# Kernel optimization log

Measured on AMD Instinct MI355X. Metric: run time of the kernel, lower is better.

## Reference

```python
import jax, jax.numpy as jnp
import numpy as np

B, S, DIM, H = 2, 1024, 512, 8
HD = DIM // H          # head_dim = 64
EPS = 1e-5
W_SCALE = 0.02         # keep activations stable (relu(gate)^2 downstream)


def causal_fft_conv(filters, x):
    """filters: [S, H]; x: [b, h, s, d]. Linear (full) convolution along s,
    truncated to the first s samples — identical to
    jax.scipy.signal.convolve(filter, seq, method='fft')[:s] per (h, d)."""
    s = x.shape[2]
    n = 2 * s  # >= 2s-1, enough for linear convolution
    f = jnp.fft.rfft(filters.T, n=n, axis=-1)          # [h, nf]
    xf = jnp.fft.rfft(x, n=n, axis=2)                  # [b, h, nf, d]
    y = jnp.fft.irfft(xf * f[None, :, :, None], n=n, axis=2)
    return y[:, :, :s, :]


def setup_inputs() -> dict:
    key = jax.random.key(0)
    ks = jax.random.split(key, 8)
    inp = {
        "x": jax.random.normal(ks[0], (B, S, DIM), dtype=jnp.float32),
        "spectral_basis": jax.random.normal(ks[1], (S, H), dtype=jnp.float32),
        "wq_w": jax.random.normal(ks[2], (DIM, DIM), dtype=jnp.float32) * W_SCALE,
        "wq_b": jnp.zeros((DIM,), jnp.float32),
        "wk_w": jax.random.normal(ks[3], (DIM, DIM), dtype=jnp.float32) * W_SCALE,
        "wk_b": jnp.zeros((DIM,), jnp.float32),
        "wv_w": jax.random.normal(ks[4], (DIM, DIM), dtype=jnp.float32) * W_SCALE,
        "wv_b": jnp.zeros((DIM,), jnp.float32),
        "wo_w": jax.random.normal(ks[5], (DIM, DIM), dtype=jnp.float32) * W_SCALE,
        "wo_b": jnp.zeros((DIM,), jnp.float32),
        "gate_w": jax.random.normal(ks[6], (HD * HD, 1), dtype=jnp.float32) * W_SCALE,
        "gate_b": jnp.zeros((1,), jnp.float32),
    }
    return inp


def reference(x, spectral_basis, wq_w, wq_b, wk_w, wk_b, wv_w, wv_b,
              wo_w, wo_b, gate_w, gate_b):
    b, s, dim = x.shape
    h = spectral_basis.shape[1]
    hd = dim // h

    def proj(w, bias):
        return (x @ w + bias).reshape(b, s, h, hd).transpose(0, 2, 1, 3)  # [b,h,s,d]

    q = proj(wq_w, wq_b)
    k = proj(wk_w, wk_b) / jnp.sqrt(jnp.asarray(hd, x.dtype))
    v = proj(wv_w, wv_b)

    k = causal_fft_conv(spectral_basis, k)
    v = causal_fft_conv(spectral_basis, v)

    # Outer-product state per step: [b, h, s, d, e]
    Z = jnp.einsum('bhsd,bhse->bhsde', v, k)

    # gate_proj: Dense(1) over flattened (d, e)
    gl = jnp.einsum('bhsde,de->bhs', Z, gate_w.reshape(hd, hd)) + gate_b[0]
    gates = jax.nn.relu(gl) ** 2 + EPS                 # [b, h, s]
    gates = gates[..., None, None]                     # [b, h, s, 1, 1]

    # Associative scan with (+, +) == cumulative sums along s
    cum_gZ = jnp.cumsum(gates * Z, axis=2)             # [b, h, s, d, e]
    cum_g = jnp.cumsum(gates, axis=2)                  # [b, h, s, 1, 1]
    attn = cum_gZ / (cum_g + EPS)

    out = jnp.einsum('bhsd,bhsde->bhse', q, attn)      # [b, h, s, e]
    nrm = jnp.linalg.norm(out, axis=3, keepdims=True)
    out = out / jnp.maximum(nrm, EPS)
    out = out.transpose(0, 2, 1, 3).reshape(b, s, dim)
    return out @ wo_w + wo_b
```

## Files before the change

### kernel.cpp

```cpp
#include <hip/hip_runtime.h>
#include <math.h>

#define B 2
#define S 1024
#define DIM 512
#define H 8
#define HD 64
#define EPS 1e-5f

typedef __attribute__((ext_vector_type(8))) short bf16x8;
typedef __attribute__((ext_vector_type(4))) float f32x4;
typedef unsigned short u16;
typedef unsigned int u32;

__device__ inline u16 f2bf(float f) {
    unsigned int u = __float_as_uint(f);
    return (u16)((u + 0x7FFF + ((u >> 16) & 1)) >> 16);
}
__device__ inline float bf2f(u16 v) {
    return __uint_as_float(((unsigned int)v) << 16);
}
__device__ inline void split2(float x, u16* hi, u16* lo) {
    u16 h = f2bf(x);
    *hi = h;
    *lo = f2bf(x - bf2f(h));
}
#define MFMA16(a, b, c) __builtin_amdgcn_mfma_f32_16x16x32_bf16((a), (b), (c), 0, 0, 0)

__device__ inline void gl16(const void* g, void* l) {
    __builtin_amdgcn_global_load_lds((const __attribute__((address_space(1))) u32*)g,
                                     (__attribute__((address_space(3))) u32*)l, 16, 0, 0);
}

__global__ void prep_k(const float* __restrict__ x,
                       const float* __restrict__ wq, const float* __restrict__ wk,
                       const float* __restrict__ wv, const float* __restrict__ wo,
                       const float* __restrict__ filt, const float* __restrict__ gw,
                       u16* __restrict__ xh, u16* __restrict__ xl,
                       u16* __restrict__ wqkvh, u16* __restrict__ wqkvl,
                       u16* __restrict__ woh, u16* __restrict__ wol,
                       u16* __restrict__ Th, u16* __restrict__ Tl,
                       u16* __restrict__ Gh, u16* __restrict__ Gl,
                       float* __restrict__ Kacc, int* __restrict__ cnt) {
    int bid = blockIdx.x, tid = threadIdx.x;
    __shared__ float T[64][65];
    if (bid < 1024) {
        int i = bid * 256 + tid;
        float4 v = ((const float4*)x)[i];
        ushort4 h, l;
        split2(v.x, &h.x, &l.x); split2(v.y, &h.y, &l.y);
        split2(v.z, &h.z, &l.z); split2(v.w, &h.w, &l.w);
        ((ushort4*)xh)[i] = h; ((ushort4*)xl)[i] = l;
    } else if (bid < 1280) {
        int q = bid - 1024;
        int z = q >> 6, rem = q & 63;
        int k0 = (rem >> 3) * 64, n0 = (rem & 7) * 64;
        const float* src = (z == 0) ? wq : (z == 1) ? wk : (z == 2) ? wv : wo;
        u16* dh = (z < 3) ? (wqkvh + (size_t)z * 512 * 512) : woh;
        u16* dl = (z < 3) ? (wqkvl + (size_t)z * 512 * 512) : wol;
        #pragma unroll
        for (int p = 0; p < 16; ++p) {
            int i = tid + 256 * p; int r = i >> 6, c = i & 63;
            T[r][c] = src[(k0 + r) * 512 + n0 + c];
        }
        __syncthreads();
        #pragma unroll
        for (int p = 0; p < 16; ++p) {
            int i = tid + 256 * p; int r = i >> 6, c = i & 63;
            size_t di = (size_t)(n0 + r) * 512 + k0 + c;
            split2(T[c][r], &dh[di], &dl[di]);
        }
    } else if (bid < 1408) {
        int q = bid - 1280;
        int h = q >> 4, delta = q & 15;
        size_t base = ((size_t)h * 16 + delta) << 12;
        #pragma unroll
        for (int p = 0; p < 16; ++p) {
            int i = tid + 256 * p;
            int t = i >> 6, s = i & 63;
            int idx = delta * 64 + t - s;
            float v = (idx >= 0 && idx < S) ? filt[idx * H + h] : 0.f;
            split2(v, &Th[base + i], &Tl[base + i]);
        }
    } else if (bid < 1920) {
        int i = (bid - 1408) * 256 + tid;
        float4 z4 = make_float4(0.f, 0.f, 0.f, 0.f);
        float4* dst = (float4*)Kacc;
        dst[i] = z4;
        dst[i + 131072] = z4;
        dst[i + 262144] = z4;
        dst[i + 393216] = z4;
    } else {
        if (tid < 16) cnt[tid] = 0;
        #pragma unroll
        for (int p = 0; p < 16; ++p) {
            int i = tid + 256 * p;
            split2(gw[i], &Gh[i], &Gl[i]);
        }
    }
}

template<int TN, int MODE>
__global__ __launch_bounds__(TN * 4) void gemm3k(
    const u16* __restrict__ Ah, const u16* __restrict__ Al,
    const u16* __restrict__ Bh, const u16* __restrict__ Bl,
    int N,
    const float* __restrict__ b0, const float* __restrict__ b1, const float* __restrict__ b2,
    float* __restrict__ outf,
    u16* __restrict__ qh, u16* __restrict__ ql,
    u16* __restrict__ kth, u16* __restrict__ ktl,
    u16* __restrict__ vth, u16* __restrict__ vtl)
{
    const int NT = TN * 4;
    __shared__ __align__(16) u16 LAh[64 * 64], LAl[64 * 64];
    __shared__ __align__(16) u16 LBh[TN * 64], LBl[TN * 64];
    int tid = threadIdx.x, l = tid & 63, wid = tid >> 6;
    int wm = wid & 1, wn = wid >> 1;
    int m0 = blockIdx.x * 64, n0 = blockIdx.y * TN;
    const u16* Abh = Ah + (size_t)m0 * 512;
    const u16* Abl = Al + (size_t)m0 * 512;
    const u16* Bbh = Bh + (size_t)n0 * 512;
    const u16* Bbl = Bl + (size_t)n0 * 512;
    int wbase = tid & ~63;
    f32x4 acc[2][2] = {};
    for (int k0s = 0; k0s < 8; ++k0s) {
        int k0 = k0s * 64;
        __syncthreads();
        #pragma unroll
        for (int i0 = 0; i0 < 512; i0 += NT) {
            int i = i0 + tid;
            int row = i >> 3, csw = (i & 7) ^ (row & 7);
            gl16(Abh + (size_t)row * 512 + k0 + csw * 8, LAh + (size_t)(i0 + wbase) * 8);
            gl16(Abl + (size_t)row * 512 + k0 + csw * 8, LAl + (size_t)(i0 + wbase) * 8);
        }
        #pragma unroll
        for (int i0 = 0; i0 < TN * 8; i0 += NT) {
            int i = i0 + tid;
            int row = i >> 3, csw = (i & 7) ^ (row & 7);
            gl16(Bbh + (size_t)row * 512 + k0 + csw * 8, LBh + (size_t)(i0 + wbase) * 8);
            gl16(Bbl + (size_t)row * 512 + k0 + csw * 8, LBl + (size_t)(i0 + wbase) * 8);
        }
        __syncthreads();
        #pragma unroll
        for (int kc = 0; kc < 2; ++kc) {
            bf16x8 ah[2], al[2], bh8[2], bl8[2];
            #pragma unroll
            for (int mi = 0; mi < 2; ++mi) {
                int ar = wm * 32 + mi * 16 + (l & 15);
                int ci = (kc * 4 + (l >> 4)) ^ (ar & 7);
                ah[mi] = *(const bf16x8*)(LAh + ar * 64 + ci * 8);
                al[mi] = *(const bf16x8*)(LAl + ar * 64 + ci * 8);
            }
            #pragma unroll
            for (int ni = 0; ni < 2; ++ni) {
                int br = wn * 32 + ni * 16 + (l & 15);
                int ci = (kc * 4 + (l >> 4)) ^ (br & 7);
                bh8[ni] = *(const bf16x8*)(LBh + br * 64 + ci * 8);
                bl8[ni] = *(const bf16x8*)(LBl + br * 64 + ci * 8);
            }
            #pragma unroll
            for (int mi = 0; mi < 2; ++mi)
                #pragma unroll
                for (int ni = 0; ni < 2; ++ni) {
                    acc[mi][ni] = MFMA16(ah[mi], bh8[ni], acc[mi][ni]);
                    acc[mi][ni] = MFMA16(ah[mi], bl8[ni], acc[mi][ni]);
                    acc[mi][ni] = MFMA16(al[mi], bh8[ni], acc[mi][ni]);
                }
        }
    }
    #pragma unroll
    for (int mi = 0; mi < 2; ++mi) {
        #pragma unroll
        for (int ni = 0; ni < 2; ++ni) {
            #pragma unroll
            for (int r = 0; r < 4; ++r) {
                int m = m0 + wm * 32 + mi * 16 + 4 * (l >> 4) + r;
                int n = n0 + wn * 32 + ni * 16 + (l & 15);
                float val = acc[mi][ni][r];
                if (MODE == 0) {
                    outf[(size_t)m * N + n] = val + b0[n];
                } else {
                    int bb = m >> 10, s = m & 1023;
                    int which = n >> 9, nn = n & 511;
                    int hh = nn >> 6, d = nn & 63;
                    int bh = bb * 8 + hh;
                    if (which == 0) {
                        val += b0[nn];
                        size_t di = ((size_t)bh * 1024 + s) * 64 + d;
                        split2(val, &qh[di], &ql[di]);
                    } else if (which == 1) {
                        val = (val + b1[nn]) * 0.125f;
                        size_t di = ((size_t)bh * 64 + d) * 1024 + s;
                        split2(val, &kth[di], &ktl[di]);
                    } else {
                        val += b2[nn];
                        size_t di = ((size_t)bh * 64 + d) * 1024 + s;
                        split2(val, &vth[di], &vtl[di]);
                    }
                }
            }
        }
    }
}

__global__ __launch_bounds__(256) void conv_part(
    const u16* __restrict__ kth, const u16* __restrict__ ktl,
    const u16* __restrict__ vth, const u16* __restrict__ vtl,
    const u16* __restrict__ Th, const u16* __restrict__ Tl,
    float* __restrict__ Kacc, float* __restrict__ Vacc)
{
    int jid = blockIdx.x, bh = blockIdx.y, h = bh & 7;
    int which = blockIdx.z;
    const u16* dhp = which ? vth : kth;
    const u16* dlp = which ? vtl : ktl;
    float* accg = which ? Vacc : Kacc;
    int tb, ch;
    if (jid < 4)       { tb = jid; ch = 0; }
    else if (jid < 12) { int q = jid - 4;  tb = 4 + (q >> 1); ch = q & 1; }
    else if (jid < 24) { int q = jid - 12; int d3 = q / 3; tb = 8 + d3; ch = q - 3 * d3; }
    else               { int q = jid - 24; tb = 12 + (q >> 2); ch = q & 3; }
    int sb0 = ch * 4, sb1 = min(sb0 + 4, tb + 1);
    int tid = threadIdx.x, wv = tid >> 6, l = tid & 63;
    __shared__ __align__(16) u16 Ash[4096], Asl[4096];
    __shared__ __align__(16) u16 Dsh[4096], Dsl[4096];
    f32x4 aD[4] = {};
    const size_t base = (size_t)bh * 64 * 1024;
    for (int sb = sb0; sb < sb1; ++sb) {
        __syncthreads();
        size_t tba = ((size_t)h * 16 + (tb - sb)) << 12;
        #pragma unroll
        for (int j = 0; j < 2; ++j) {
            int row = (j * 4 + wv) * 8 + (l >> 3);
            int csw = (l & 7) ^ (row & 7);
            int lo = (j * 4 + wv) * 512;
            gl16(Th + tba + row * 64 + csw * 8, Ash + lo);
            gl16(Tl + tba + row * 64 + csw * 8, Asl + lo);
            size_t gb = base + (size_t)row * 1024 + sb * 64 + csw * 8;
            gl16(dhp + gb, Dsh + lo);
            gl16(dlp + gb, Dsl + lo);
        }
        __syncthreads();
        #pragma unroll
        for (int seg = 0; seg < 3; ++seg) {
            const u16* Ase = (seg < 2) ? Ash : Asl;
            const u16* Dse = (seg == 1) ? Dsl : Dsh;
            #pragma unroll
            for (int kc = 0; kc < 2; ++kc) {
                int ar = 16 * wv + (l & 15);
                int acb = (kc * 64 + (l >> 4) * 16) ^ ((ar & 7) << 4);
                bf16x8 a = *(const bf16x8*)((const char*)(Ase + ar * 64) + acb);
                #pragma unroll
                for (int cf = 0; cf < 4; ++cf) {
                    int br = cf * 16 + (l & 15);
                    int bcb = (kc * 64 + (l >> 4) * 16) ^ ((br & 7) << 4);
                    bf16x8 bd = *(const bf16x8*)((const char*)(Dse + br * 64) + bcb);
                    aD[cf] = MFMA16(a, bd, aD[cf]);
                }
            }
        }
    }
    #pragma unroll
    for (int cf = 0; cf < 4; ++cf) {
        #pragma unroll
        for (int r = 0; r < 4; ++r) {
            int tl_ = 16 * wv + 4 * (l >> 4) + r;
            int d = cf * 16 + (l & 15);
            size_t oi = ((size_t)bh * 1024 + tb * 64 + tl_) * 64 + d;
            atomicAdd(&accg[oi], aD[cf][r]);
        }
    }
}

__global__ void conv_fin(const float* __restrict__ Kacc, const float* __restrict__ Vacc,
                         const u16* __restrict__ Gh, const u16* __restrict__ Gl,
                         const float* __restrict__ gb,
                         u16* __restrict__ kcth, u16* __restrict__ kctl,
                         u16* __restrict__ vcrh, u16* __restrict__ vcrl,
                         u16* __restrict__ vcth, u16* __restrict__ vctl,
                         float* __restrict__ g, float* __restrict__ cumg,
                         int* __restrict__ cnt) {
    int sc = blockIdx.x, bh = blockIdx.y;
    int tid = threadIdx.x, tx = tid & 63, ty = tid >> 6;
    int w = ty, l = tx;
    __shared__ float Kt[64][65], Vt[64][65];
    __shared__ float wtot[4];
    __shared__ int lastFlag;
    for (int i = tid; i < 4096; i += 256) {
        int r = i >> 6, c = i & 63;
        Kt[r][c] = Kacc[(((size_t)bh * 1024) + sc * 64 + r) * 64 + c];
        Vt[r][c] = Vacc[(((size_t)bh * 1024) + sc * 64 + r) * 64 + c];
    }
    __syncthreads();
    f32x4 tac[4] = {};
    #pragma unroll
    for (int kc = 0; kc < 2; ++kc) {
        int ar = 16 * w + (l & 15);
        int ac = kc * 32 + (l >> 4) * 8;
        bf16x8 ah, al;
        #pragma unroll
        for (int q = 0; q < 8; ++q) {
            float kv = Kt[ar][ac + q];
            u16 hi = f2bf(kv);
            ah[q] = (short)hi;
            al[q] = (short)f2bf(kv - bf2f(hi));
        }
        #pragma unroll
        for (int cf = 0; cf < 4; ++cf) {
            int br = cf * 16 + (l & 15);
            bf16x8 gh8 = *(const bf16x8*)&Gh[br * 64 + ac];
            bf16x8 gl8 = *(const bf16x8*)&Gl[br * 64 + ac];
            tac[cf] = MFMA16(ah, gh8, tac[cf]);
            tac[cf] = MFMA16(ah, gl8, tac[cf]);
            tac[cf] = MFMA16(al, gh8, tac[cf]);
        }
    }
    float gbias = gb[0];
    #pragma unroll
    for (int r = 0; r < 4; ++r) {
        int row = 16 * w + 4 * (l >> 4) + r;
        float pr = 0.f;
        #pragma unroll
        for (int cf = 0; cf < 4; ++cf) {
            int d = cf * 16 + (l & 15);
            pr += tac[cf][r] * Vt[row][d];
        }
        #pragma unroll
        for (int off = 1; off < 16; off <<= 1) pr += __shfl_xor(pr, off);
        if ((l & 15) == 0) {
            float gg = fmaxf(pr + gbias, 0.f);
            g[(size_t)bh * 1024 + sc * 64 + row] = gg * gg + EPS;
        }
    }
    #pragma unroll
    for (int it = 0; it < 16; ++it) {
        int r = it * 4 + ty;
        size_t ri = ((size_t)bh * 1024 + sc * 64 + r) * 64 + tx;
        split2(Vt[r][tx], &vcrh[ri], &vcrl[ri]);
    }
    #pragma unroll
    for (int it = 0; it < 16; ++it) {
        int d = it * 4 + ty;
        size_t ti = ((size_t)bh * 64 + d) * 1024 + sc * 64 + tx;
        split2(Kt[tx][d], &kcth[ti], &kctl[ti]);
        split2(Vt[tx][d], &vcth[ti], &vctl[ti]);
    }
    __threadfence();
    if (tid == 0) lastFlag = (atomicAdd(&cnt[bh], 1) == 15) ? 1 : 0;
    __syncthreads();
    if (lastFlag) {
        __threadfence();
        int ll = tid & 63, wv = tid >> 6;
        float4 v = ((const float4*)(g + (size_t)bh * 1024))[tid];
        float p0 = v.x, p1 = p0 + v.y, p2 = p1 + v.z, p3 = p2 + v.w;
        float t = p3, scn = t;
        #pragma unroll
        for (int off = 1; off < 64; off <<= 1) {
            float u = __shfl_up(scn, off);
            if (ll >= off) scn += u;
        }
        if (ll == 63) wtot[wv] = scn;
        __syncthreads();
        float bse = scn - t;
        for (int w2 = 0; w2 < wv; ++w2) bse += wtot[w2];
        float4 o = make_float4(bse + p0, bse + p1, bse + p2, bse + p3);
        ((float4*)(cumg + (size_t)bh * 1024))[tid] = o;
    }
}

__global__ void states_mfma(const u16* __restrict__ kcth, const u16* __restrict__ kctl,
                            const u16* __restrict__ vcth, const u16* __restrict__ vctl,
                            const float* __restrict__ g, float* __restrict__ Mst) {
    int j = blockIdx.x, bh = blockIdx.y;
    int tid = threadIdx.x, w = tid >> 6, l = tid & 63;
    __shared__ __align__(16) u16 Ash[64][72], Asl[64][72], Bsh[64][72], Bsl[64][72];
    __shared__ float gs[64];
    if (tid < 64) gs[tid] = g[(size_t)bh * 1024 + j * 64 + tid];
    __syncthreads();
    #pragma unroll
    for (int p = 0; p < 2; ++p) {
        int i = tid + 256 * p; int r = i >> 3, c8 = (i & 7) * 8;
        bf16x8 kh8 = *(const bf16x8*)&kcth[((size_t)bh * 64 + r) * 1024 + j * 64 + c8];
        bf16x8 kl8 = *(const bf16x8*)&kctl[((size_t)bh * 64 + r) * 1024 + j * 64 + c8];
        #pragma unroll
        for (int q = 0; q < 8; ++q) {
            float f = (bf2f((u16)kh8[q]) + bf2f((u16)kl8[q])) * gs[c8 + q];
            split2(f, &Ash[r][c8 + q], &Asl[r][c8 + q]);
        }
        *(bf16x8*)&Bsh[r][c8] = *(const bf16x8*)&vcth[((size_t)bh * 64 + r) * 1024 + j * 64 + c8];
        *(bf16x8*)&Bsl[r][c8] = *(const bf16x8*)&vctl[((size_t)bh * 64 + r) * 1024 + j * 64 + c8];
    }
    __syncthreads();
    f32x4 acc[4] = {};
    #pragma unroll
    for (int kc = 0; kc < 2; ++kc) {
        int ar = 16 * w + (l & 15), ac = kc * 32 + (l >> 4) * 8;
        bf16x8 ah = *(const bf16x8*)&Ash[ar][ac];
        bf16x8 al = *(const bf16x8*)&Asl[ar][ac];
        #pragma unroll
        for (int cf = 0; cf < 4; ++cf) {
            int br = cf * 16 + (l & 15);
            bf16x8 bh_ = *(const bf16x8*)&Bsh[br][ac];
            bf16x8 bl_ = *(const bf16x8*)&Bsl[br][ac];
            acc[cf] = MFMA16(ah, bh_, acc[cf]);
            acc[cf] = MFMA16(ah, bl_, acc[cf]);
            acc[cf] = MFMA16(al, bh_, acc[cf]);
        }
    }
    #pragma unroll
    for (int cf = 0; cf < 4; ++cf) {
        #pragma unroll
        for (int r = 0; r < 4; ++r) {
            int e = 16 * w + 4 * (l >> 4) + r;
            int d = cf * 16 + (l & 15);
            Mst[(((size_t)bh * 16 + j) * 64 + e) * 64 + d] = acc[cf][r];
        }
    }
}

__global__ void attn_mfma(const u16* __restrict__ qh, const u16* __restrict__ ql,
                          const float* __restrict__ Mst,
                          const u16* __restrict__ vcrh, const u16* __restrict__ vcrl,
                          const u16* __restrict__ kcth, const u16* __restrict__ kctl,
                          const float* __restrict__ g, const float* __restrict__ cumg,
                          u16* __restrict__ yh, u16* __restrict__ yl) {
    int tb = blockIdx.x, bh = blockIdx.y;
    int b = bh >> 3, h = bh & 7;
    int tid = threadIdx.x, w = tid >> 6, l = tid & 63;
    __shared__ __align__(16) u16 buf[6][64][72];
    __shared__ float gl_s[64], cg_s[64];
    float pref[16];
    #pragma unroll
    for (int p = 0; p < 16; ++p) pref[p] = 0.f;
    for (int j = 0; j < tb; ++j) {
        const float* Mb = Mst + ((size_t)(bh * 16 + j)) * 4096;
        #pragma unroll
        for (int p = 0; p < 16; ++p) pref[p] += Mb[tid + 256 * p];
    }
    #pragma unroll
    for (int p = 0; p < 2; ++p) {
        int i = tid + 256 * p; int r = i >> 3, c8 = (i & 7) * 8;
        size_t rowi = ((size_t)bh * 1024 + tb * 64 + r) * 64 + c8;
        *(bf16x8*)&buf[0][r][c8] = *(const bf16x8*)&qh[rowi];
        *(bf16x8*)&buf[1][r][c8] = *(const bf16x8*)&ql[rowi];
        *(bf16x8*)&buf[4][r][c8] = *(const bf16x8*)&vcrh[rowi];
        *(bf16x8*)&buf[5][r][c8] = *(const bf16x8*)&vcrl[rowi];
    }
    #pragma unroll
    for (int p = 0; p < 16; ++p) {
        int pos = tid + 256 * p;
        int r = pos >> 6, c = pos & 63;
        split2(pref[p], &buf[2][r][c], &buf[3][r][c]);
    }
    if (tid < 64) {
        gl_s[tid] = g[(size_t)bh * 1024 + tb * 64 + tid];
        cg_s[tid] = cumg[(size_t)bh * 1024 + tb * 64 + tid];
    }
    __syncthreads();
    f32x4 o[4] = {}, sc[4] = {};
    #pragma unroll
    for (int kc = 0; kc < 2; ++kc) {
        int ar = 16 * w + (l & 15), ac = kc * 32 + (l >> 4) * 8;
        bf16x8 ah = *(const bf16x8*)&buf[0][ar][ac];
        bf16x8 al = *(const bf16x8*)&buf[1][ar][ac];
        #pragma unroll
        for (int cf = 0; cf < 4; ++cf) {
            int br = cf * 16 + (l & 15);
            bf16x8 bph = *(const bf16x8*)&buf[2][br][ac];
            bf16x8 bpl = *(const bf16x8*)&buf[3][br][ac];
            bf16x8 bvh = *(const bf16x8*)&buf[4][br][ac];
            bf16x8 bvl = *(const bf16x8*)&buf[5][br][ac];
            o[cf] = MFMA16(ah, bph, o[cf]);
            o[cf] = MFMA16(ah, bpl, o[cf]);
            o[cf] = MFMA16(al, bph, o[cf]);
            sc[cf] = MFMA16(ah, bvh, sc[cf]);
            sc[cf] = MFMA16(ah, bvl, sc[cf]);
            sc[cf] = MFMA16(al, bvh, sc[cf]);
        }
    }
    __syncthreads();
    #pragma unroll
    for (int cf = 0; cf < 4; ++cf) {
        int s = cf * 16 + (l & 15);
        float gsv = gl_s[s];
        #pragma unroll
        for (int r = 0; r < 4; ++r) {
            int t = 16 * w + 4 * (l >> 4) + r;
            float v = (s <= t) ? sc[cf][r] * gsv : 0.f;
            split2(v, &buf[2][t][s], &buf[3][t][s]);
        }
    }
    #pragma unroll
    for (int p = 0; p < 2; ++p) {
        int i = tid + 256 * p; int r = i >> 3, c8 = (i & 7) * 8;
        size_t ti = ((size_t)bh * 64 + r) * 1024 + tb * 64 + c8;
        *(bf16x8*)&buf[4][r][c8] = *(const bf16x8*)&kcth[ti];
        *(bf16x8*)&buf[5][r][c8] = *(const bf16x8*)&kctl[ti];
    }
    __syncthreads();
    #pragma unroll
    for (int kc = 0; kc < 2; ++kc) {
        int ar = 16 * w + (l & 15), ac = kc * 32 + (l >> 4) * 8;
        bf16x8 ah = *(const bf16x8*)&buf[2][ar][ac];
        bf16x8 al = *(const bf16x8*)&buf[3][ar][ac];
        #pragma unroll
        for (int cf = 0; cf < 4; ++cf) {
            int br = cf * 16 + (l & 15);
            bf16x8 bh_ = *(const bf16x8*)&buf[4][br][ac];
            bf16x8 bl_ = *(const bf16x8*)&buf[5][br][ac];
            o[cf] = MFMA16(ah, bh_, o[cf]);
            o[cf] = MFMA16(ah, bl_, o[cf]);
            o[cf] = MFMA16(al, bh_, o[cf]);
        }
    }
    #pragma unroll
    for (int r = 0; r < 4; ++r) {
        int tl_ = 16 * w + 4 * (l >> 4) + r;
        float inv = 1.f / (cg_s[tl_] + EPS);
        float vv[4]; float sq = 0.f;
        #pragma unroll
        for (int cf = 0; cf < 4; ++cf) { vv[cf] = o[cf][r] * inv; sq += vv[cf] * vv[cf]; }
        #pragma unroll
        for (int off = 1; off < 16; off <<= 1) sq += __shfl_xor(sq, off);
        float scale = 1.f / fmaxf(sqrtf(sq), EPS);
        int tg = tb * 64 + tl_;
        #pragma unroll
        for (int cf = 0; cf < 4; ++cf) {
            int e = cf * 16 + (l & 15);
            size_t yi = ((size_t)b * 1024 + tg) * 512 + h * 64 + e;
            split2(vv[cf] * scale, &yh[yi], &yl[yi]);
        }
    }
}

extern "C" void kernel_launch(void* const* d_in, const int* in_sizes, int n_in,
                              void* d_out, int out_size, void* d_ws, size_t ws_size,
                              hipStream_t stream) {
    const float* x    = (const float*)d_in[0];
    const float* sbas = (const float*)d_in[1];
    const float* wq_w = (const float*)d_in[2];
    const float* wq_b = (const float*)d_in[3];
    const float* wk_w = (const float*)d_in[4];
    const float* wk_b = (const float*)d_in[5];
    const float* wv_w = (const float*)d_in[6];
    const float* wv_b = (const float*)d_in[7];
    const float* wo_w = (const float*)d_in[8];
    const float* wo_b = (const float*)d_in[9];
    const float* gw   = (const float*)d_in[10];
    const float* gb   = (const float*)d_in[11];
    float* out = (float*)d_out;

    char* p = (char*)d_ws;
    auto carve = [&](size_t bytes) { char* r = p; p += (bytes + 255) & ~(size_t)255; return r; };
    const size_t T2 = (size_t)2048 * 512 * 2;
    u16* xh = (u16*)carve(T2);      u16* xl = (u16*)carve(T2);
    u16* wqkvh = (u16*)carve((size_t)1536 * 512 * 2);
    u16* wqkvl = (u16*)carve((size_t)1536 * 512 * 2);
    u16* woh = (u16*)carve((size_t)512 * 512 * 2);
    u16* wol = (u16*)carve((size_t)512 * 512 * 2);
    u16* qh_ = (u16*)carve(T2);     u16* ql_ = (u16*)carve(T2);
    u16* kth_ = (u16*)carve(T2);    u16* ktl_ = (u16*)carve(T2);
    u16* vth_ = (u16*)carve(T2);    u16* vtl_ = (u16*)carve(T2);
    u16* Tth = (u16*)carve((size_t)8 * 16 * 4096 * 2);
    u16* Ttl = (u16*)carve((size_t)8 * 16 * 4096 * 2);
    u16* Gh_ = (u16*)carve(4096 * 2);
    u16* Gl_ = (u16*)carve(4096 * 2);
    float* Kacc = (float*)carve((size_t)16 * 1024 * 64 * 4);
    float* Vacc = (float*)carve((size_t)16 * 1024 * 64 * 4);
    u16* kcth_ = (u16*)carve(T2);   u16* kctl_ = (u16*)carve(T2);
    u16* vcrh_ = (u16*)carve(T2);   u16* vcrl_ = (u16*)carve(T2);
    u16* vcth_ = (u16*)carve(T2);   u16* vctl_ = (u16*)carve(T2);
    float* gbuf = (float*)carve((size_t)16 * 1024 * 4);
    float* cumg = (float*)carve((size_t)16 * 1024 * 4);
    float* Mst  = (float*)carve((size_t)16 * 16 * 4096 * 4);
    u16* yh_ = (u16*)carve(T2);     u16* yl_ = (u16*)carve(T2);
    int* cnt  = (int*)carve(64 * 4);

    prep_k<<<1921, 256, 0, stream>>>(x, wq_w, wk_w, wv_w, wo_w, sbas, gw,
                                     xh, xl, wqkvh, wqkvl, woh, wol, Tth, Ttl,
                                     Gh_, Gl_, Kacc, cnt);
    gemm3k<128, 1><<<dim3(32, 12), 512, 0, stream>>>(xh, xl, wqkvh, wqkvl, 1536,
                                                     wq_b, wk_b, wv_b, nullptr,
                                                     qh_, ql_, kth_, ktl_, vth_, vtl_);
    conv_part<<<dim3(40, 16, 2), 256, 0, stream>>>(kth_, ktl_, vth_, vtl_, Tth, Ttl, Kacc, Vacc);
    conv_fin<<<dim3(16, 16), 256, 0, stream>>>(Kacc, Vacc, Gh_, Gl_, gb,
                                               kcth_, kctl_, vcrh_, vcrl_, vcth_, vctl_,
                                               gbuf, cumg, cnt);
    states_mfma<<<dim3(16, 16), 256, 0, stream>>>(kcth_, kctl_, vcth_, vctl_, gbuf, Mst);
    attn_mfma<<<dim3(16, 16), 256, 0, stream>>>(qh_, ql_, Mst, vcrh_, vcrl_,
                                                kcth_, kctl_, gbuf, cumg, yh_, yl_);
    gemm3k<64, 0><<<dim3(32, 8), 256, 0, stream>>>(yh_, yl_, woh, wol, 512,
                                                   wo_b, nullptr, nullptr, out,
                                                   nullptr, nullptr, nullptr, nullptr, nullptr, nullptr);
}
```

Baseline: 191.1 us.

## Fuse per-chunk state computation into conv_fin and widen block to 512 threads

The states_mfma kernel is folded into conv_fin, which now computes the gated K^T V chunk state straight from the fp32 K/V tiles already held in shared memory. This removes one kernel launch and the global re-read of the split bf16 K/V arrays. The block grows to 512 threads so the gate projection and the state MFMAs are split across two column halves, with partial gate sums combined through shared memory. In exchange, each thread does more bf16 hi/lo splitting in registers, and the last-block cumulative-sum path has to guard threads beyond 256.

```diff
diff --git a/kernel.cpp b/kernel.cpp
--- a/kernel.cpp
+++ b/kernel.cpp
@@ -271,30 +271,34 @@
     }
 }
 
-__global__ void conv_fin(const float* __restrict__ Kacc, const float* __restrict__ Vacc,
-                         const u16* __restrict__ Gh, const u16* __restrict__ Gl,
-                         const float* __restrict__ gb,
-                         u16* __restrict__ kcth, u16* __restrict__ kctl,
-                         u16* __restrict__ vcrh, u16* __restrict__ vcrl,
-                         u16* __restrict__ vcth, u16* __restrict__ vctl,
-                         float* __restrict__ g, float* __restrict__ cumg,
-                         int* __restrict__ cnt) {
+__global__ __launch_bounds__(512) void conv_fin(
+        const float* __restrict__ Kacc, const float* __restrict__ Vacc,
+        const u16* __restrict__ Gh, const u16* __restrict__ Gl,
+        const float* __restrict__ gb,
+        u16* __restrict__ kcth, u16* __restrict__ kctl,
+        u16* __restrict__ vcrh, u16* __restrict__ vcrl,
+        u16* __restrict__ vcth, u16* __restrict__ vctl,
+        float* __restrict__ g, float* __restrict__ cumg,
+        float* __restrict__ Mst, int* __restrict__ cnt) {
     int sc = blockIdx.x, bh = blockIdx.y;
-    int tid = threadIdx.x, tx = tid & 63, ty = tid >> 6;
-    int w = ty, l = tx;
+    int tid = threadIdx.x, l = tid & 63;
+    int w = tid >> 6;
+    int rg = w & 3, chh = w >> 2;
     __shared__ float Kt[64][65], Vt[64][65];
+    __shared__ float pg[2][64];
+    __shared__ float gsh[64];
     __shared__ float wtot[4];
     __shared__ int lastFlag;
-    for (int i = tid; i < 4096; i += 256) {
+    for (int i = tid; i < 4096; i += 512) {
         int r = i >> 6, c = i & 63;
         Kt[r][c] = Kacc[(((size_t)bh * 1024) + sc * 64 + r) * 64 + c];
         Vt[r][c] = Vacc[(((size_t)bh * 1024) + sc * 64 + r) * 64 + c];
     }
     __syncthreads();
-    f32x4 tac[4] = {};
+    f32x4 tac[2] = {};
     #pragma unroll
     for (int kc = 0; kc < 2; ++kc) {
-        int ar = 16 * w + (l & 15);
+        int ar = 16 * rg + (l & 15);
         int ac = kc * 32 + (l >> 4) * 8;
         bf16x8 ah, al;
         #pragma unroll
@@ -305,52 +309,98 @@
             al[q] = (short)f2bf(kv - bf2f(hi));
         }
         #pragma unroll
-        for (int cf = 0; cf < 4; ++cf) {
-            int br = cf * 16 + (l & 15);
+        for (int cfi = 0; cfi < 2; ++cfi) {
+            int br = (chh * 2 + cfi) * 16 + (l & 15);
             bf16x8 gh8 = *(const bf16x8*)&Gh[br * 64 + ac];
             bf16x8 gl8 = *(const bf16x8*)&Gl[br * 64 + ac];
-            tac[cf] = MFMA16(ah, gh8, tac[cf]);
-            tac[cf] = MFMA16(ah, gl8, tac[cf]);
-            tac[cf] = MFMA16(al, gh8, tac[cf]);
-        }
-    }
+            tac[cfi] = MFMA16(ah, gh8, tac[cfi]);
+            tac[cfi] = MFMA16(ah, gl8, tac[cfi]);
+            tac[cfi] = MFMA16(al, gh8, tac[cfi]);
+        }
+    }
+    #pragma unroll
+    for (int r = 0; r < 4; ++r) {
+        int row = 16 * rg + 4 * (l >> 4) + r;
+        float pr = 0.f;
+        #pragma unroll
+        for (int cfi = 0; cfi < 2; ++cfi) {
+            int d = (chh * 2 + cfi) * 16 + (l & 15);
+            pr += tac[cfi][r] * Vt[row][d];
+        }
+        #pragma unroll
+        for (int off = 1; off < 16; off <<= 1) pr += __shfl_xor(pr, off);
+        if ((l & 15) == 0) pg[chh][row] = pr;
+    }
+    __syncthreads();
     float gbias = gb[0];
-    #pragma unroll
-    for (int r = 0; r < 4; ++r) {
-        int row = 16 * w + 4 * (l >> 4) + r;
-        float pr = 0.f;
-        #pragma unroll
-        for (int cf = 0; cf < 4; ++cf) {
-            int d = cf * 16 + (l & 15);
-            pr += tac[cf][r] * Vt[row][d];
-        }
-        #pragma unroll
-        for (int off = 1; off < 16; off <<= 1) pr += __shfl_xor(pr, off);
-        if ((l & 15) == 0) {
-            float gg = fmaxf(pr + gbias, 0.f);
-            g[(size_t)bh * 1024 + sc * 64 + row] = gg * gg + EPS;
-        }
-    }
-    #pragma unroll
-    for (int it = 0; it < 16; ++it) {
-        int r = it * 4 + ty;
-        size_t ri = ((size_t)bh * 1024 + sc * 64 + r) * 64 + tx;
-        split2(Vt[r][tx], &vcrh[ri], &vcrl[ri]);
-    }
-    #pragma unroll
-    for (int it = 0; it < 16; ++it) {
-        int d = it * 4 + ty;
-        size_t ti = ((size_t)bh * 64 + d) * 1024 + sc * 64 + tx;
-        split2(Kt[tx][d], &kcth[ti], &kctl[ti]);
-        split2(Vt[tx][d], &vcth[ti], &vctl[ti]);
+    if (tid < 64) {
+        float gg = fmaxf(pg[0][tid] + pg[1][tid] + gbias, 0.f);
+        float gv = gg * gg + EPS;
+        gsh[tid] = gv;
+        g[(size_t)bh * 1024 + sc * 64 + tid] = gv;
+    }
+    __syncthreads();
+    {
+        f32x4 mac[2] = {};
+        #pragma unroll
+        for (int kc = 0; kc < 2; ++kc) {
+            int are = 16 * rg + (l & 15);
+            int ac = kc * 32 + (l >> 4) * 8;
+            bf16x8 ah, al;
+            #pragma unroll
+            for (int q = 0; q < 8; ++q) {
+                float f = gsh[ac + q] * Kt[ac + q][are];
+                u16 hi = f2bf(f);
+                ah[q] = (short)hi;
+                al[q] = (short)f2bf(f - bf2f(hi));
+            }
+            #pragma unroll
+            for (int cfi = 0; cfi < 2; ++cfi) {
+                int brd = (chh * 2 + cfi) * 16 + (l & 15);
+                bf16x8 bh8, bl8;
+                #pragma unroll
+                for (int q = 0; q < 8; ++q) {
+                    float f = Vt[ac + q][brd];
+                    u16 hi = f2bf(f);
+                    bh8[q] = (short)hi;
+                    bl8[q] = (short)f2bf(f - bf2f(hi));
+                }
+                mac[cfi] = MFMA16(ah, bh8, mac[cfi]);
+                mac[cfi] = MFMA16(ah, bl8, mac[cfi]);
+                mac[cfi] = MFMA16(al, bh8, mac[cfi]);
+            }
+        }
+        #pragma unroll
+        for (int cfi = 0; cfi < 2; ++cfi) {
+            #pragma unroll
+            for (int r = 0; r < 4; ++r) {
+                int e = 16 * rg + 4 * (l >> 4) + r;
+                int d = (chh * 2 + cfi) * 16 + (l & 15);
+                Mst[(((size_t)bh * 16 + sc) * 64 + e) * 64 + d] = mac[cfi][r];
+            }
+        }
+    }
+    #pragma unroll
+    for (int it = 0; it < 8; ++it) {
+        int r = it * 8 + w;
+        size_t ri = ((size_t)bh * 1024 + sc * 64 + r) * 64 + l;
+        split2(Vt[r][l], &vcrh[ri], &vcrl[ri]);
+    }
+    #pragma unroll
+    for (int it = 0; it < 8; ++it) {
+        int d = it * 8 + w;
+        size_t ti = ((size_t)bh * 64 + d) * 1024 + sc * 64 + l;
+        split2(Kt[l][d], &kcth[ti], &kctl[ti]);
+        split2(Vt[l][d], &vcth[ti], &vctl[ti]);
     }
     __threadfence();
     if (tid == 0) lastFlag = (atomicAdd(&cnt[bh], 1) == 15) ? 1 : 0;
     __syncthreads();
     if (lastFlag) {
         __threadfence();
-        int ll = tid & 63, wv = tid >> 6;
-        float4 v = ((const float4*)(g + (size_t)bh * 1024))[tid];
+        int ll = tid & 63;
+        float4 v = (tid < 256) ? ((const float4*)(g + (size_t)bh * 1024))[tid]
+                               : make_float4(0.f, 0.f, 0.f, 0.f);
         float p0 = v.x, p1 = p0 + v.y, p2 = p1 + v.z, p3 = p2 + v.w;
         float t = p3, scn = t;
         #pragma unroll
@@ -358,61 +408,14 @@
             float u = __shfl_up(scn, off);
             if (ll >= off) scn += u;
         }
-        if (ll == 63) wtot[wv] = scn;
+        if (tid < 256 && ll == 63) wtot[tid >> 6] = scn;
         __syncthreads();
-        float bse = scn - t;
-        for (int w2 = 0; w2 < wv; ++w2) bse += wtot[w2];
-        float4 o = make_float4(bse + p0, bse + p1, bse + p2, bse + p3);
-        ((float4*)(cumg + (size_t)bh * 1024))[tid] = o;
-    }
-}
-
-__global__ void states_mfma(const u16* __restrict__ kcth, const u16* __restrict__ kctl,
-                            const u16* __restrict__ vcth, const u16* __restrict__ vctl,
-                            const float* __restrict__ g, float* __restrict__ Mst) {
-    int j = blockIdx.x, bh = blockIdx.y;
-    int tid = threadIdx.x, w = tid >> 6, l = tid & 63;
-    __shared__ __align__(16) u16 Ash[64][72], Asl[64][72], Bsh[64][72], Bsl[64][72];
-    __shared__ float gs[64];
-    if (tid < 64) gs[tid] = g[(size_t)bh * 1024 + j * 64 + tid];
-    __syncthreads();
-    #pragma unroll
-    for (int p = 0; p < 2; ++p) {
-        int i = tid + 256 * p; int r = i >> 3, c8 = (i & 7) * 8;
-        bf16x8 kh8 = *(const bf16x8*)&kcth[((size_t)bh * 64 + r) * 1024 + j * 64 + c8];
-        bf16x8 kl8 = *(const bf16x8*)&kctl[((size_t)bh * 64 + r) * 1024 + j * 64 + c8];
-        #pragma unroll
-        for (int q = 0; q < 8; ++q) {
-            float f = (bf2f((u16)kh8[q]) + bf2f((u16)kl8[q])) * gs[c8 + q];
-            split2(f, &Ash[r][c8 + q], &Asl[r][c8 + q]);
-        }
-        *(bf16x8*)&Bsh[r][c8] = *(const bf16x8*)&vcth[((size_t)bh * 64 + r) * 1024 + j * 64 + c8];
-        *(bf16x8*)&Bsl[r][c8] = *(const bf16x8*)&vctl[((size_t)bh * 64 + r) * 1024 + j * 64 + c8];
-    }
-    __syncthreads();
-    f32x4 acc[4] = {};
-    #pragma unroll
-    for (int kc = 0; kc < 2; ++kc) {
-        int ar = 16 * w + (l & 15), ac = kc * 32 + (l >> 4) * 8;
-        bf16x8 ah = *(const bf16x8*)&Ash[ar][ac];
-        bf16x8 al = *(const bf16x8*)&Asl[ar][ac];
-        #pragma unroll
-        for (int cf = 0; cf < 4; ++cf) {
-            int br = cf * 16 + (l & 15);
-            bf16x8 bh_ = *(const bf16x8*)&Bsh[br][ac];
-            bf16x8 bl_ = *(const bf16x8*)&Bsl[br][ac];
-            acc[cf] = MFMA16(ah, bh_, acc[cf]);
-            acc[cf] = MFMA16(ah, bl_, acc[cf]);
-            acc[cf] = MFMA16(al, bh_, acc[cf]);
-        }
-    }
-    #pragma unroll
-    for (int cf = 0; cf < 4; ++cf) {
-        #pragma unroll
-        for (int r = 0; r < 4; ++r) {
-            int e = 16 * w + 4 * (l >> 4) + r;
-            int d = cf * 16 + (l & 15);
-            Mst[(((size_t)bh * 16 + j) * 64 + e) * 64 + d] = acc[cf][r];
+        if (tid < 256) {
+            int wv = tid >> 6;
+            float bse = scn - t;
+            for (int w2 = 0; w2 < wv; ++w2) bse += wtot[w2];
+            float4 o = make_float4(bse + p0, bse + p1, bse + p2, bse + p3);
+            ((float4*)(cumg + (size_t)bh * 1024))[tid] = o;
         }
     }
 }
@@ -582,10 +585,9 @@
                                                      wq_b, wk_b, wv_b, nullptr,
                                                      qh_, ql_, kth_, ktl_, vth_, vtl_);
     conv_part<<<dim3(40, 16, 2), 256, 0, stream>>>(kth_, ktl_, vth_, vtl_, Tth, Ttl, Kacc, Vacc);
-    conv_fin<<<dim3(16, 16), 256, 0, stream>>>(Kacc, Vacc, Gh_, Gl_, gb,
+    conv_fin<<<dim3(16, 16), 512, 0, stream>>>(Kacc, Vacc, Gh_, Gl_, gb,
                                                kcth_, kctl_, vcrh_, vcrl_, vcth_, vctl_,
-                                               gbuf, cumg, cnt);
-    states_mfma<<<dim3(16, 16), 256, 0, stream>>>(kcth_, kctl_, vcth_, vctl_, gbuf, Mst);
+                                               gbuf, cumg, Mst, cnt);
     attn_mfma<<<dim3(16, 16), 256, 0, stream>>>(qh_, ql_, Mst, vcrh_, vcrl_,
                                                 kcth_, kctl_, gbuf, cumg, yh_, yl_);
     gemm3k<64, 0><<<dim3(32, 8), 256, 0, stream>>>(yh_, yl_, woh, wol, 512,
```

Result: slower. 215.5 us (+12.8%).
